# Kernel optimization log

Hardware: AMD Instinct MI355X
Metric: run time of the kernel (lower is better)

Reference implementation:

```python
import jax, jax.numpy as jnp
import numpy as np

EPS = 1e-8  # F.cosine_similarity default eps


def setup_inputs() -> dict:
    key = jax.random.key(0)
    k1, k2, k3 = jax.random.split(key, 3)
    C, S, Q, D_IN, Z_DIM = 256, 5, 64, 1024, 128
    xs = jax.random.normal(k1, (C, S, D_IN), dtype=jnp.float32)
    xq = jax.random.normal(k2, (C, Q, D_IN), dtype=jnp.float32)
    W = jax.random.normal(k3, (D_IN, Z_DIM), dtype=jnp.float32) / np.sqrt(D_IN)
    return {"xs": xs, "xq": xq, "W": W}


def _protonet_loss(xs, xq, W):
    C, S, D = xs.shape
    Q = xq.shape[1]
    # encoder (linear) applied to concatenated support+query, as in the original
    x = jnp.concatenate([xs.reshape(C * S, D), xq.reshape(C * Q, D)], axis=0)
    z = x @ W                                   # [C*(S+Q), Zd]
    Zd = z.shape[-1]
    z_proto = z[: C * S].reshape(C, S, Zd).mean(axis=1)   # [C, Zd]
    zq = z[C * S:]                                        # [C*Q, Zd]
    # squared euclidean distance (GEMM form, avoids [CQ, C, Zd] intermediate)
    d2 = (jnp.sum(zq * zq, axis=-1, keepdims=True)
          + jnp.sum(z_proto * z_proto, axis=-1)[None, :]
          - 2.0 * (zq @ z_proto.T))                       # [C*Q, C]
    lp = d2.reshape(C, Q, C)                              # label_predicts
    # leave-one-out: for each class i drop column i -> [C, Q, C-1]
    loo_idx = np.stack([np.delete(np.arange(C), i) for i in range(C)])  # [C, C-1]
    idx = jnp.broadcast_to(jnp.asarray(loo_idx)[:, None, :], (C, Q, C - 1))
    loo = jnp.take_along_axis(lp, idx, axis=2)            # [C, Q, C-1]
    # pairwise cosine similarity between query rows j<k, per class
    nrm = jnp.maximum(jnp.linalg.norm(loo, axis=-1), EPS)
    a = loo / nrm[..., None]
    sim = jnp.einsum('cqd,ckd->cqk', a, a)                # [C, Q, Q]
    pair_mask = jnp.triu(jnp.ones((Q, Q), dtype=bool), 1)
    n_pairs = C * (Q * (Q - 1) // 2)
    cos_loss = jnp.sum(jnp.where(pair_mask[None], sim, 0.0)) / n_pairs
    # log_softmax over prototype axis; accuracy vs diagonal targets
    log_p_y = jax.nn.log_softmax(-d2, axis=1).reshape(C, Q, C)
    y_hat = jnp.argmax(log_p_y, axis=2)                   # [C, Q]
    acc = jnp.mean((y_hat == jnp.arange(C)[:, None]).astype(jnp.float32))
    # original overwrites loss_val with the cosine-similarity loss
    return cos_loss, acc


def reference(xs, xq, W):
    return _protonet_loss(xs, xq, W)
```

## Files before the change

### kernel.cpp

```cpp
#include <hip/hip_runtime.h>
#include <stdint.h>


typedef __attribute__((ext_vector_type(8))) short s8v;
typedef __attribute__((ext_vector_type(4))) float f32x4;

__device__ __forceinline__ short f2bf(float f) {
  union { float f; unsigned u; } v; v.f = f;
  unsigned r = (v.u + 0x7fffu + ((v.u >> 16) & 1u)) >> 16;
  return (short)r;
}

__device__ __forceinline__ void async16(const void* g, void* s) {
  typedef __attribute__((address_space(3))) uint32_t lds_t;
  typedef const __attribute__((address_space(1))) uint32_t glb_t;
  __builtin_amdgcn_global_load_lds((glb_t*)(uintptr_t)g,
                                   (lds_t*)(uint32_t)(uintptr_t)s, 16, 0, 0);
}

__global__ __launch_bounds__(256) void k_prep(
    const float* __restrict__ xs, const float* __restrict__ W,
    float* __restrict__ xbar, unsigned short* __restrict__ Wt,
    float* __restrict__ out) {
  __shared__ unsigned short T[128 * 68];
  const int tid = threadIdx.x;
  if (blockIdx.x < 256) {
    const int c = blockIdx.x;
    if (c == 0 && tid < 2) out[tid] = 0.0f;
    const float* b = xs + (size_t)c * 5120;
    for (int e = tid; e < 1024; e += 256) {
      float s = b[e] + b[1024 + e] + b[2048 + e] + b[3072 + e] + b[4096 + e];
      xbar[(size_t)c * 1024 + e] = s * 0.2f;
    }
  } else {
    const int kb = (blockIdx.x - 256) * 64;
#pragma unroll
    for (int s = 0; s < 8; ++s) {
      int idx = tid + s * 256;
      int kr = idx >> 5, n4 = idx & 31;
      float4 v = *(const float4*)(W + (size_t)(kb + kr) * 128 + n4 * 4);
      T[(n4 * 4 + 0) * 68 + kr] = (unsigned short)f2bf(v.x);
      T[(n4 * 4 + 1) * 68 + kr] = (unsigned short)f2bf(v.y);
      T[(n4 * 4 + 2) * 68 + kr] = (unsigned short)f2bf(v.z);
      T[(n4 * 4 + 3) * 68 + kr] = (unsigned short)f2bf(v.w);
    }
    __syncthreads();
#pragma unroll
    for (int s = 0; s < 8; ++s) {
      int idx = tid + s * 256;
      int n = idx >> 4, k4 = idx & 15;
      ushort4 o;
      o.x = T[n * 68 + k4 * 4 + 0];
      o.y = T[n * 68 + k4 * 4 + 1];
      o.z = T[n * 68 + k4 * 4 + 2];
      o.w = T[n * 68 + k4 * 4 + 3];
      *(ushort4*)(Wt + (size_t)n * 1024 + kb + k4 * 4) = o;
    }
  }
}

__global__ __launch_bounds__(256, 2) void k_gemm_z(
    const float* __restrict__ xbar, const float* __restrict__ xq,
    const unsigned short* __restrict__ Wt,
    unsigned short* __restrict__ zb, float* __restrict__ n2) {
  __shared__ __align__(16) char SM[2][32768];
  const int tid = threadIdx.x;
  const int w = tid >> 6, l = tid & 63, ln = l & 15, qd = l >> 4;
  const int mb = blockIdx.x * 64;
  const float* abase = (mb < 256) ? (xbar + (size_t)mb * 1024)
                                  : (xq + (size_t)(mb - 256) * 1024);
  const float* as[4];
#pragma unroll
  for (int i = 0; i < 4; ++i)
    as[i] = abase + (size_t)(w * 16 + ln) * 1024 + (i >> 1) * 32 + qd * 8 + (i & 1) * 4;
  const unsigned short* bs[4];
  bs[0] = Wt + (size_t)(2 * w * 16 + ln) * 1024 + qd * 8;
  bs[1] = bs[0] + 32;
  bs[2] = bs[0] + 16 * 1024;
  bs[3] = bs[2] + 32;

  f32x4 acc[8] = {};

#pragma unroll
  for (int i = 0; i < 4; ++i)
    async16(as[i], SM[0] + (w * 4 + i) * 1024);
#pragma unroll
  for (int i = 0; i < 4; ++i)
    async16(bs[i], SM[0] + 16384 + (w * 4 + i) * 1024);

  for (int kt = 0; kt < 16; ++kt) {
    const int buf = kt & 1;
    __syncthreads();
    if (kt < 15) {
#pragma unroll
      for (int i = 0; i < 4; ++i)
        async16(as[i] + (kt + 1) * 64, SM[buf ^ 1] + (w * 4 + i) * 1024);
#pragma unroll
      for (int i = 0; i < 4; ++i)
        async16(bs[i] + (kt + 1) * 64, SM[buf ^ 1] + 16384 + (w * 4 + i) * 1024);
    }
#pragma unroll
    for (int ks = 0; ks < 2; ++ks) {
      f32x4 alo = *(const f32x4*)(SM[buf] + (w * 4 + ks * 2 + 0) * 1024 + l * 16);
      f32x4 ahi = *(const f32x4*)(SM[buf] + (w * 4 + ks * 2 + 1) * 1024 + l * 16);
      s8v af = { f2bf(alo[0]), f2bf(alo[1]), f2bf(alo[2]), f2bf(alo[3]),
                 f2bf(ahi[0]), f2bf(ahi[1]), f2bf(ahi[2]), f2bf(ahi[3]) };
#pragma unroll
      for (int t = 0; t < 8; ++t) {
        s8v bf = *(const s8v*)(SM[buf] + 16384 + (t * 2 + ks) * 1024 + l * 16);
        acc[t] = __builtin_amdgcn_mfma_f32_16x16x32_bf16(af, bf, acc[t], 0, 0, 0);
      }
    }
  }
#pragma unroll
  for (int p = 0; p < 4; ++p) {
    const int grow = mb + w * 16 + qd * 4 + p;
    float sp = 0.0f;
#pragma unroll
    for (int t = 0; t < 8; ++t) {
      float v = acc[t][p];
      zb[(size_t)grow * 128 + t * 16 + ln] = (unsigned short)f2bf(v);
      sp += v * v;
    }
    sp += __shfl_xor(sp, 1);
    sp += __shfl_xor(sp, 2);
    sp += __shfl_xor(sp, 4);
    sp += __shfl_xor(sp, 8);
    if (ln == 0) n2[grow] = sp;
  }
}

__global__ __launch_bounds__(256, 1) void k_d2red(
    const unsigned short* __restrict__ zb, const float* __restrict__ n2,
    float* __restrict__ out) {
  __shared__ float Dt[256 * 65];
  __shared__ float rv[256];
  __shared__ int   ri[256];
  __shared__ float rss[256];
  __shared__ float invn[64];
  __shared__ float sred[4];
  __shared__ float s_tc, s_aq2, s_corr;
  const int tid = threadIdx.x;
  const int c = blockIdx.x;
  const int w = tid >> 6, lane = tid & 63, ln = lane & 15, qd = lane >> 4;

  f32x4 acc[16] = {};
  const unsigned short* Az = zb + (size_t)(256 + c * 64 + w * 16 + ln) * 128;
  s8v af[4];
#pragma unroll
  for (int kt = 0; kt < 4; ++kt) af[kt] = *(const s8v*)(Az + kt * 32 + qd * 8);
#pragma unroll
  for (int t = 0; t < 16; ++t) {
    const unsigned short* Bz = zb + (size_t)(t * 16 + ln) * 128 + qd * 8;
    s8v bf0 = *(const s8v*)(Bz + 0 * 32);
    s8v bf1 = *(const s8v*)(Bz + 1 * 32);
    s8v bf2 = *(const s8v*)(Bz + 2 * 32);
    s8v bf3 = *(const s8v*)(Bz + 3 * 32);
    acc[t] = __builtin_amdgcn_mfma_f32_16x16x32_bf16(af[0], bf0, acc[t], 0, 0, 0);
    acc[t] = __builtin_amdgcn_mfma_f32_16x16x32_bf16(af[1], bf1, acc[t], 0, 0, 0);
    acc[t] = __builtin_amdgcn_mfma_f32_16x16x32_bf16(af[2], bf2, acc[t], 0, 0, 0);
    acc[t] = __builtin_amdgcn_mfma_f32_16x16x32_bf16(af[3], bf3, acc[t], 0, 0, 0);
  }
#pragma unroll
  for (int p = 0; p < 4; ++p) {
    int qloc = w * 16 + qd * 4 + p;
    float qn = n2[256 + c * 64 + qloc];
#pragma unroll
    for (int t = 0; t < 16; ++t) {
      int j = t * 16 + ln;
      Dt[j * 65 + qloc] = qn + n2[j] - 2.0f * acc[t][p];
    }
  }
  __syncthreads();

  {
    const int q = tid & 63, jb = (tid >> 6) * 64;
    float mn = 3.4e38f; int mi = 0; float ss = 0.0f;
    for (int jj = 0; jj < 64; ++jj) {
      int j = jb + jj;
      float f = Dt[j * 65 + q];
      ss += f * f;
      if (f < mn) { mn = f; mi = j; }
    }
    rv[tid] = mn; ri[tid] = mi; rss[tid] = ss;
  }
  __syncthreads();
  if (tid < 64) {
    float bm = rv[tid]; int bi = ri[tid]; float ss = rss[tid];
    for (int hh = 1; hh < 4; ++hh) {
      float v = rv[hh * 64 + tid];
      ss += rss[hh * 64 + tid];
      if (v < bm) { bm = v; bi = ri[hh * 64 + tid]; }
    }
    float col = Dt[c * 65 + tid];
    float loo2 = fmaxf(ss - col * col, 0.0f);
    float nrm = fmaxf(sqrtf(loo2), 1e-8f);
    float inv = 1.0f / nrm;
    invn[tid] = inv;
    float aq2 = loo2 * inv * inv;
    float corr = (bi == c) ? 1.0f : 0.0f;
    for (int m = 1; m < 64; m <<= 1) {
      aq2 += __shfl_xor(aq2, m);
      corr += __shfl_xor(corr, m);
    }
    if (tid == 0) { s_aq2 = aq2; s_corr = corr; }
  }
  __syncthreads();
  float t = 0.0f;
  for (int qq = 0; qq < 64; ++qq) t += Dt[tid * 65 + qq] * invn[qq];
  if (tid == c) s_tc = t;
  float t2 = t * t;
  for (int m = 1; m < 64; m <<= 1) t2 += __shfl_xor(t2, m);
  if ((tid & 63) == 0) sred[tid >> 6] = t2;
  __syncthreads();
  if (tid == 0) {
    float S2 = sred[0] + sred[1] + sred[2] + sred[3];
    float bs = 0.5f * (S2 - s_tc * s_tc - s_aq2);
    atomicAdd(&out[0], bs * (1.0f / 516096.0f));
    atomicAdd(&out[1], s_corr * (1.0f / 16384.0f));
  }
}

extern "C" void kernel_launch(void* const* d_in, const int* in_sizes, int n_in,
                              void* d_out, int out_size, void* d_ws, size_t ws_size,
                              hipStream_t stream) {
  const float* xs = (const float*)d_in[0];
  const float* xq = (const float*)d_in[1];
  const float* W  = (const float*)d_in[2];
  float* out = (float*)d_out;

  float* ws = (float*)d_ws;
  float* xbar = ws;
  unsigned short* Wt = (unsigned short*)(xbar + 262144);
  unsigned short* zb = Wt + 131072;
  float* n2 = (float*)(zb + (size_t)16640 * 128);

  k_prep<<<dim3(272), dim3(256), 0, stream>>>(xs, W, xbar, Wt, out);
  k_gemm_z<<<dim3(260), dim3(256), 0, stream>>>(xbar, xq, Wt, zb, n2);
  k_d2red<<<dim3(256), dim3(256), 0, stream>>>(zb, n2, out);
}
```

Baseline: 139.2 us.

## Halve GEMM M-tile to 32 rows and split N across warps

The z-projection GEMM now uses 32-row tiles instead of 64, doubling the grid from 260 to 520 blocks so more CUs have work. Each warp computes a 16x64 quadrant (row group by column half), and partial row norms are combined through shared memory before being written. The cost is that the W tile is reloaded twice as often per row, and each block does an extra sync and reduction step.

```diff
diff --git a/kernel.cpp b/kernel.cpp
--- a/kernel.cpp
+++ b/kernel.cpp
@@ -63,70 +63,83 @@
     const float* __restrict__ xbar, const float* __restrict__ xq,
     const unsigned short* __restrict__ Wt,
     unsigned short* __restrict__ zb, float* __restrict__ n2) {
-  __shared__ __align__(16) char SM[2][32768];
+  __shared__ __align__(16) char SM[2][24576];
+  __shared__ float P[4][16];
   const int tid = threadIdx.x;
   const int w = tid >> 6, l = tid & 63, ln = l & 15, qd = l >> 4;
-  const int mb = blockIdx.x * 64;
+  const int rg = w & 1, ch = w >> 1;
+  const int mb = blockIdx.x * 32;
   const float* abase = (mb < 256) ? (xbar + (size_t)mb * 1024)
                                   : (xq + (size_t)(mb - 256) * 1024);
-  const float* as[4];
+  const float* as[2];
+#pragma unroll
+  for (int i = 0; i < 2; ++i) {
+    int ar = w * 2 + i;
+    int r16g = ar >> 2, ks = (ar >> 1) & 1, e = ar & 1;
+    as[i] = abase + (size_t)(r16g * 16 + ln) * 1024 + ks * 32 + qd * 8 + e * 4;
+  }
+  const unsigned short* bs[4];
+#pragma unroll
+  for (int i = 0; i < 4; ++i) {
+    int br = w * 4 + i;
+    int t = br >> 1, ks = br & 1;
+    bs[i] = Wt + (size_t)(t * 16 + ln) * 1024 + ks * 32 + qd * 8;
+  }
+
+  f32x4 acc[4] = {};
+
+#pragma unroll
+  for (int i = 0; i < 2; ++i)
+    async16(as[i], SM[0] + (w * 2 + i) * 1024);
 #pragma unroll
   for (int i = 0; i < 4; ++i)
-    as[i] = abase + (size_t)(w * 16 + ln) * 1024 + (i >> 1) * 32 + qd * 8 + (i & 1) * 4;
-  const unsigned short* bs[4];
-  bs[0] = Wt + (size_t)(2 * w * 16 + ln) * 1024 + qd * 8;
-  bs[1] = bs[0] + 32;
-  bs[2] = bs[0] + 16 * 1024;
-  bs[3] = bs[2] + 32;
-
-  f32x4 acc[8] = {};
-
-#pragma unroll
-  for (int i = 0; i < 4; ++i)
-    async16(as[i], SM[0] + (w * 4 + i) * 1024);
-#pragma unroll
-  for (int i = 0; i < 4; ++i)
-    async16(bs[i], SM[0] + 16384 + (w * 4 + i) * 1024);
+    async16(bs[i], SM[0] + 8192 + (w * 4 + i) * 1024);
 
   for (int kt = 0; kt < 16; ++kt) {
     const int buf = kt & 1;
     __syncthreads();
     if (kt < 15) {
 #pragma unroll
+      for (int i = 0; i < 2; ++i)
+        async16(as[i] + (kt + 1) * 64, SM[buf ^ 1] + (w * 2 + i) * 1024);
+#pragma unroll
       for (int i = 0; i < 4; ++i)
-        async16(as[i] + (kt + 1) * 64, SM[buf ^ 1] + (w * 4 + i) * 1024);
-#pragma unroll
-      for (int i = 0; i < 4; ++i)
-        async16(bs[i] + (kt + 1) * 64, SM[buf ^ 1] + 16384 + (w * 4 + i) * 1024);
+        async16(bs[i] + (kt + 1) * 64, SM[buf ^ 1] + 8192 + (w * 4 + i) * 1024);
     }
 #pragma unroll
     for (int ks = 0; ks < 2; ++ks) {
-      f32x4 alo = *(const f32x4*)(SM[buf] + (w * 4 + ks * 2 + 0) * 1024 + l * 16);
-      f32x4 ahi = *(const f32x4*)(SM[buf] + (w * 4 + ks * 2 + 1) * 1024 + l * 16);
+      f32x4 alo = *(const f32x4*)(SM[buf] + (rg * 4 + ks * 2 + 0) * 1024 + l * 16);
+      f32x4 ahi = *(const f32x4*)(SM[buf] + (rg * 4 + ks * 2 + 1) * 1024 + l * 16);
       s8v af = { f2bf(alo[0]), f2bf(alo[1]), f2bf(alo[2]), f2bf(alo[3]),
                  f2bf(ahi[0]), f2bf(ahi[1]), f2bf(ahi[2]), f2bf(ahi[3]) };
 #pragma unroll
-      for (int t = 0; t < 8; ++t) {
-        s8v bf = *(const s8v*)(SM[buf] + 16384 + (t * 2 + ks) * 1024 + l * 16);
+      for (int t = 0; t < 4; ++t) {
+        int br = (ch * 4 + t) * 2 + ks;
+        s8v bf = *(const s8v*)(SM[buf] + 8192 + br * 1024 + l * 16);
         acc[t] = __builtin_amdgcn_mfma_f32_16x16x32_bf16(af, bf, acc[t], 0, 0, 0);
       }
     }
   }
 #pragma unroll
   for (int p = 0; p < 4; ++p) {
-    const int grow = mb + w * 16 + qd * 4 + p;
+    const int grow = mb + rg * 16 + qd * 4 + p;
     float sp = 0.0f;
 #pragma unroll
-    for (int t = 0; t < 8; ++t) {
+    for (int t = 0; t < 4; ++t) {
       float v = acc[t][p];
-      zb[(size_t)grow * 128 + t * 16 + ln] = (unsigned short)f2bf(v);
+      zb[(size_t)grow * 128 + ch * 64 + t * 16 + ln] = (unsigned short)f2bf(v);
       sp += v * v;
     }
     sp += __shfl_xor(sp, 1);
     sp += __shfl_xor(sp, 2);
     sp += __shfl_xor(sp, 4);
     sp += __shfl_xor(sp, 8);
-    if (ln == 0) n2[grow] = sp;
+    if (ln == 0) P[w][qd * 4 + p] = sp;
+  }
+  __syncthreads();
+  if (tid < 32) {
+    const int r = tid >> 4, i = tid & 15;
+    n2[mb + r * 16 + i] = P[r][i] + P[r + 2][i];
   }
 }
 
@@ -236,6 +249,6 @@
   float* n2 = (float*)(zb + (size_t)16640 * 128);
 
   k_prep<<<dim3(272), dim3(256), 0, stream>>>(xs, W, xbar, Wt, out);
-  k_gemm_z<<<dim3(260), dim3(256), 0, stream>>>(xbar, xq, Wt, zb, n2);
+  k_gemm_z<<<dim3(520), dim3(256), 0, stream>>>(xbar, xq, Wt, zb, n2);
   k_d2red<<<dim3(256), dim3(256), 0, stream>>>(zb, n2, out);
 }
```

After: 143.6 us. 1.03x slower.
